# Performance work log

Measured on AMD Instinct MI355X. Metric: run time of the kernel, lower is better.

Reference implementation:

```python
import jax, jax.numpy as jnp
import numpy as np

L, S, B, E, H, M = 1024, 1024, 4, 1024, 16, 256
HD = E // H


def embed_rotary(x, cos, sin):
    # x: (B, T, E); interleaved rotary as in RotaryPositionEncoding.embed_rotary
    x2 = jnp.stack([-x[..., 1::2], x[..., ::2]], axis=-1).reshape(x.shape)
    return x * cos + x2 * sin


def setup_inputs() -> dict:
    key = jax.random.key(0)
    ks = jax.random.split(key, 12)
    return {
        "query": jax.random.normal(ks[0], (L, B, E), jnp.float32),
        "key": jax.random.normal(ks[1], (S, B, E), jnp.float32),
        "value": jax.random.normal(ks[2], (S, B, E), jnp.float32),
        "in_proj_weight": jax.random.normal(ks[3], (3 * E, E), jnp.float32) * (E ** -0.5),
        "in_proj_bias": jax.random.normal(ks[4], (3 * E,), jnp.float32) * 0.02,
        "out_proj_weight": jax.random.normal(ks[5], (E, E), jnp.float32) * (E ** -0.5),
        "out_proj_bias": jax.random.normal(ks[6], (E,), jnp.float32) * 0.02,
        "q_pe": jax.random.uniform(ks[7], (B, L, E, 2), jnp.float32),
        "kv_pe": jax.random.uniform(ks[8], (B, S, E, 2), jnp.float32),
        "k_mem": jax.random.normal(ks[9], (M, B, E), jnp.float32),
        "v_mem": jax.random.normal(ks[10], (M, B, E), jnp.float32),
        "gate_attn": jax.random.normal(ks[11], (H,), jnp.float32),
    }


def reference(query, key, value, in_proj_weight, in_proj_bias, out_proj_weight,
              out_proj_bias, q_pe, kv_pe, k_mem, v_mem, gate_attn):
    scaling = HD ** -0.5
    # separate q/k/v projections from slices of in_proj (q!=k!=v branch)
    q = query @ in_proj_weight[:E].T + in_proj_bias[:E]
    k = key @ in_proj_weight[E:2 * E].T + in_proj_bias[E:2 * E]
    v = value @ in_proj_weight[2 * E:].T + in_proj_bias[2 * E:]
    q = q * scaling
    # rotary PE applied on (B, T, E) layout
    q = embed_rotary(q.swapaxes(0, 1), q_pe[..., 0], q_pe[..., 1]).swapaxes(0, 1)
    k = embed_rotary(k.swapaxes(0, 1), kv_pe[..., 0], kv_pe[..., 1]).swapaxes(0, 1)
    # (T, B, E) -> (B*H, T, HD)
    qh = q.reshape(L, B * H, HD).swapaxes(0, 1)
    kh = k.reshape(S, B * H, HD).swapaxes(0, 1)
    vh = v.reshape(S, B * H, HD).swapaxes(0, 1)
    scores = jnp.einsum('bld,bsd->bls', qh, kh)  # (B*H, L, S)
    # slot-competition: softmax over queries, renormalize over keys
    w = jax.nn.softmax(scores, axis=-2) + 1e-8
    w = w / jnp.sum(w, axis=-1, keepdims=True)
    attn = jnp.einsum('bls,bsd->bld', w, vh)
    # memory attention (k_mem/v_mem already projected, shape (M, B, E))
    kmh = k_mem.reshape(M, B * H, HD).swapaxes(0, 1)
    vmh = v_mem.reshape(M, B * H, HD).swapaxes(0, 1)
    wm = jax.nn.softmax(jnp.einsum('bld,bmd->blm', qh, kmh), axis=-1)
    attn_mem = jnp.einsum('blm,bmd->bld', wm, vmh)
    # per-head sigmoid gating between memory and main outputs
    gate = jnp.tile(jax.nn.sigmoid(gate_attn), B)[:, None, None]  # (B*H,1,1)
    attn = gate * attn_mem + (1.0 - gate) * attn
    out = attn.swapaxes(0, 1).reshape(L, B, E) @ out_proj_weight.T + out_proj_bias
    return out
```

## Files before the change

### kernel.cpp

```cpp
#include <hip/hip_runtime.h>
#include <hip/hip_bf16.h>

typedef __bf16 bf16;
typedef __bf16 bf16x8 __attribute__((ext_vector_type(8)));
typedef float f32x4 __attribute__((ext_vector_type(4)));

#define LL 1024
#define SS 1024
#define BB 4
#define EE 1024
#define HH 16
#define MM 256
#define HD 64
#define BH 64

__device__ __forceinline__ f32x4 mfma16(bf16x8 a, bf16x8 b, f32x4 c) {
  return __builtin_amdgcn_mfma_f32_16x16x32_bf16(a, b, c, 0, 0, 0);
}

__device__ __forceinline__ void gload_lds16(const bf16* g, bf16* l) {
  __builtin_amdgcn_global_load_lds(
      (const __attribute__((address_space(1))) unsigned int*)(g),
      (__attribute__((address_space(3))) unsigned int*)(l), 16, 0, 0);
}

#define RING_BARRIER(N)                                         \
  do {                                                          \
    asm volatile("s_waitcnt vmcnt(" #N ")" ::: "memory");       \
    __builtin_amdgcn_s_barrier();                               \
    __builtin_amdgcn_sched_barrier(0);                          \
  } while (0)

__device__ __forceinline__ bf16x8 cvt8(const float* p) {
  const f32x4 lo = *reinterpret_cast<const f32x4*>(p);
  const f32x4 hi = *reinterpret_cast<const f32x4*>(p + 4);
  bf16x8 r;
  r[0] = (bf16)lo[0]; r[1] = (bf16)lo[1]; r[2] = (bf16)lo[2]; r[3] = (bf16)lo[3];
  r[4] = (bf16)hi[0]; r[5] = (bf16)hi[1]; r[6] = (bf16)hi[2]; r[7] = (bf16)hi[3];
  return r;
}

__global__ __launch_bounds__(256) void cvt_all_kernel(
    const float* __restrict__ ipw, const float* __restrict__ opw,
    const float* __restrict__ k_mem, const float* __restrict__ query,
    const float* __restrict__ key_i, const float* __restrict__ value,
    bf16* __restrict__ wb, bf16* __restrict__ opwb, bf16* __restrict__ kmemb,
    bf16* __restrict__ xq, bf16* __restrict__ xk, bf16* __restrict__ xv) {
  const int bid = blockIdx.x, tid = threadIdx.x;
  if (bid >= 6656) {
    const size_t i8 = ((size_t)(bid - 6656) * 256 + tid) * 8;
    const int e = (int)(i8 & (EE - 1));
    const int row = (int)(i8 >> 10);
    const int s = row >> 2, b = row & 3;
    *reinterpret_cast<bf16x8*>(xv + (((size_t)b * SS + s) << 10) + e) = cvt8(value + i8);
    return;
  }
  const float* src; bf16* dst; int base;
  if (bid < 1536)      { src = ipw;   dst = wb;    base = 0; }
  else if (bid < 2048) { src = opw;   dst = opwb;  base = 1536; }
  else if (bid < 2560) { src = k_mem; dst = kmemb; base = 2048; }
  else if (bid < 4608) { src = query; dst = xq;    base = 2560; }
  else                 { src = key_i; dst = xk;    base = 4608; }
  const size_t i = ((size_t)(bid - base) * 256 + tid) * 8;
  *reinterpret_cast<bf16x8*>(dst + i) = cvt8(src + i);
}

__global__ __launch_bounds__(256) void vmt_kernel(
    const float* __restrict__ v_mem, bf16* __restrict__ vmT) {
  __shared__ float sm[64][65];
  const int bid = blockIdx.x;
  const int bh = bid >> 2, mc = bid & 3;
  const int b = bh >> 4, h = bh & 15;
  const int m0 = mc * 64;
  const int tid = threadIdx.x;
  const int d = tid & 63, mi = tid >> 6;
#pragma unroll
  for (int mm = mi; mm < 64; mm += 4)
    sm[mm][d] = v_mem[((size_t)(m0 + mm) * BB + b) * EE + h * 64 + d];
  __syncthreads();
  const int mw = tid & 63, di = tid >> 6;
#pragma unroll
  for (int dd = di; dd < 64; dd += 4)
    vmT[((size_t)bh * HD + dd) * MM + m0 + mw] = (bf16)sm[mw][dd];
}

__global__ __launch_bounds__(256) void rope_kernel(
    bf16* __restrict__ qh, bf16* __restrict__ kh,
    const float* __restrict__ q_pe, const float* __restrict__ kv_pe) {
  const size_t CP = (size_t)BH * LL * HD / 8;
  size_t gi = (size_t)blockIdx.x * 256 + threadIdx.x;
  bf16* x; const float* pe;
  if (gi < CP) { x = qh; pe = q_pe; }
  else         { x = kh; pe = kv_pe; gi -= CP; }
  const int d8 = gi & 7;
  const int t  = (int)((gi >> 3) & (LL - 1));
  const int bh = (int)(gi >> 13);
  const int b = bh >> 4, h = bh & 15;
  bf16* xp = x + gi * 8;
  const float* pp = pe + (((size_t)b * LL + t) * EE + h * 64 + d8 * 8) * 2;
  bf16x8 v = *reinterpret_cast<const bf16x8*>(xp);
  const f32x4 p0 = *reinterpret_cast<const f32x4*>(pp);
  const f32x4 p1 = *reinterpret_cast<const f32x4*>(pp + 4);
  const f32x4 p2 = *reinterpret_cast<const f32x4*>(pp + 8);
  const f32x4 p3 = *reinterpret_cast<const f32x4*>(pp + 12);
  float cs[8], sn[8], xv[8];
  cs[0]=p0[0]; sn[0]=p0[1]; cs[1]=p0[2]; sn[1]=p0[3];
  cs[2]=p1[0]; sn[2]=p1[1]; cs[3]=p1[2]; sn[3]=p1[3];
  cs[4]=p2[0]; sn[4]=p2[1]; cs[5]=p2[2]; sn[5]=p2[3];
  cs[6]=p3[0]; sn[6]=p3[1]; cs[7]=p3[2]; sn[7]=p3[3];
#pragma unroll
  for (int j = 0; j < 8; ++j) xv[j] = (float)v[j];
  bf16x8 o;
#pragma unroll
  for (int j = 0; j < 8; j += 2) {
    o[j]     = (bf16)(xv[j]     * cs[j]     - xv[j + 1] * sn[j]);
    o[j + 1] = (bf16)(xv[j + 1] * cs[j + 1] + xv[j]     * sn[j + 1]);
  }
  *reinterpret_cast<bf16x8*>(xp) = o;
}

__global__ __launch_bounds__(256) void gemm3_kernel(
    const bf16* __restrict__ xq, const bf16* __restrict__ xk,
    const bf16* __restrict__ xv, const bf16* __restrict__ wb,
    const float* __restrict__ ipb, bf16* __restrict__ qh,
    bf16* __restrict__ kh, bf16* __restrict__ vhT) {
  __shared__ bf16 As[3][4096];
  __shared__ bf16 Bs[3][4096];
  const int tid = threadIdx.x;
  const int wv = tid >> 6, lane = tid & 63;
  const int lrow = lane & 15, lkg = lane >> 4;
  const int wr = wv >> 1, wc = wv & 1;
  const int n = (blockIdx.x & 7) * 96 + (blockIdx.x >> 3);
  const int which = n >> 8, sub = n & 255;

  const bf16* X; const bf16* W;
  int rowA0, colB0;
  if (which == 2) {
    X = wb + 2 * (size_t)EE * EE;
    W = xv;
    rowA0 = (sub & 7) * 128;
    colB0 = (sub >> 3) * 128;
  } else {
    X = (which == 0) ? xq : xk;
    W = wb + (size_t)which * EE * EE;
    rowA0 = (sub >> 3) * 128;
    colB0 = (sub & 7) * 128;
  }

  const f32x4 zero = {0.f, 0.f, 0.f, 0.f};
  f32x4 acc[4][4];
#pragma unroll
  for (int i = 0; i < 4; ++i)
#pragma unroll
    for (int j = 0; j < 4; ++j) acc[i][j] = zero;

  auto stage = [&](int buf, int k0) {
#pragma unroll
    for (int t = 0; t < 2; ++t) {
      const int i = wv * 2 + t;
      const int slot = i * 64 + lane;
      const int srow = slot & 127, sk8 = slot >> 7;
      gload_lds16(X + (size_t)(rowA0 + srow) * EE + k0 + sk8 * 8, &As[buf][i * 512]);
      gload_lds16(W + (size_t)(colB0 + srow) * EE + k0 + sk8 * 8, &Bs[buf][i * 512]);
    }
  };

  stage(0, 0);
  stage(1, 32);
  RING_BARRIER(4);
  for (int ks = 0; ks < 32; ++ks) {
    const int buf = ks % 3;
    if (ks + 2 < 32) stage((ks + 2) % 3, (ks + 2) * 32);
    bf16x8 av[4], bv[4];
#pragma unroll
    for (int i = 0; i < 4; ++i) {
      av[i] = *reinterpret_cast<const bf16x8*>(&As[buf][lkg * 1024 + (wr * 64 + i * 16 + lrow) * 8]);
      bv[i] = *reinterpret_cast<const bf16x8*>(&Bs[buf][lkg * 1024 + (wc * 64 + i * 16 + lrow) * 8]);
    }
#pragma unroll
    for (int mt = 0; mt < 4; ++mt)
#pragma unroll
      for (int nt = 0; nt < 4; ++nt)
        acc[mt][nt] = mfma16(av[mt], bv[nt], acc[mt][nt]);
    if (ks + 2 < 32) { RING_BARRIER(4); } else { RING_BARRIER(0); }
  }

  if (which == 2) {
#pragma unroll
    for (int mt = 0; mt < 4; ++mt) {
#pragma unroll
      for (int r = 0; r < 4; ++r) {
        const int rowg = rowA0 + wr * 64 + mt * 16 + lkg * 4 + r;
        const float bs = ipb[2 * EE + rowg];
        const int h = rowg >> 6, d = rowg & 63;
#pragma unroll
        for (int nt = 0; nt < 4; ++nt) {
          const int c = colB0 + wc * 64 + nt * 16 + lrow;
          const int b = c >> 10, s = c & (SS - 1);
          vhT[(((size_t)(b * HH + h)) * HD + d) * SS + s] = (bf16)(acc[mt][nt][r] + bs);
        }
      }
    }
  } else {
#pragma unroll
    for (int nt = 0; nt < 4; ++nt) {
      const int col = colB0 + wc * 64 + nt * 16 + lrow;
      const float bs = ipb[which * EE + col];
      const int h = col >> 6, d = col & 63;
#pragma unroll
      for (int mt = 0; mt < 4; ++mt) {
#pragma unroll
        for (int r = 0; r < 4; ++r) {
          const int rowg = rowA0 + wr * 64 + mt * 16 + lkg * 4 + r;
          const int t = rowg >> 2;
          const int b = rowg & 3;
          float v = acc[mt][nt][r] + bs;
          if (which == 0) v *= 0.125f;
          const int bh = b * HH + h;
          if (which == 1)
            kh[((size_t)bh * LL + t) * HD + d] = (bf16)v;
          else
            qh[((size_t)bh * LL + t) * HD + d] = (bf16)v;
        }
      }
    }
  }
}

__global__ __launch_bounds__(256) void gemm_out_kernel(
    const bf16* __restrict__ Xb, const bf16* __restrict__ W,
    const float* __restrict__ bias, float* __restrict__ outf) {
  __shared__ bf16 As[3][4096];
  __shared__ bf16 Bs[3][2048];
  const int tid = threadIdx.x;
  const int wv = tid >> 6, lane = tid & 63;
  const int lrow = lane & 15, lkg = lane >> 4;
  const int wr = wv >> 1, wc = wv & 1;
  const int n = (blockIdx.x & 7) * 64 + (blockIdx.x >> 3);
  const int rowt = n >> 4, colt = n & 15;
  const int rowA0 = rowt * 128, colB0 = colt * 64;

  const f32x4 zero = {0.f, 0.f, 0.f, 0.f};
  f32x4 acc[4][2];
#pragma unroll
  for (int i = 0; i < 4; ++i)
#pragma unroll
    for (int j = 0; j < 2; ++j) acc[i][j] = zero;

  auto stage = [&](int buf, int k0) {
#pragma unroll
    for (int t = 0; t < 2; ++t) {
      const int i = wv * 2 + t;
      const int slot = i * 64 + lane;
      const int srow = slot & 127, sk8 = slot >> 7;
      gload_lds16(Xb + (size_t)(rowA0 + srow) * EE + k0 + sk8 * 8, &As[buf][i * 512]);
    }
    {
      const int slot = wv * 64 + lane;
      const int srow = slot & 63, sk8 = slot >> 6;
      gload_lds16(W + (size_t)(colB0 + srow) * EE + k0 + sk8 * 8, &Bs[buf][wv * 512]);
    }
  };

  stage(0, 0);
  stage(1, 32);
  RING_BARRIER(3);
  for (int ks = 0; ks < 32; ++ks) {
    const int buf = ks % 3;
    if (ks + 2 < 32) stage((ks + 2) % 3, (ks + 2) * 32);
    bf16x8 av[4], bv[2];
#pragma unroll
    for (int i = 0; i < 4; ++i)
      av[i] = *reinterpret_cast<const bf16x8*>(&As[buf][lkg * 1024 + (wr * 64 + i * 16 + lrow) * 8]);
#pragma unroll
    for (int j = 0; j < 2; ++j)
      bv[j] = *reinterpret_cast<const bf16x8*>(&Bs[buf][lkg * 512 + (wc * 32 + j * 16 + lrow) * 8]);
#pragma unroll
    for (int mt = 0; mt < 4; ++mt)
#pragma unroll
      for (int nt = 0; nt < 2; ++nt)
        acc[mt][nt] = mfma16(av[mt], bv[nt], acc[mt][nt]);
    if (ks + 2 < 32) { RING_BARRIER(3); } else { RING_BARRIER(0); }
  }

#pragma unroll
  for (int nt = 0; nt < 2; ++nt) {
    const int col = colB0 + wc * 32 + nt * 16 + lrow;
    const float bs = bias[col];
#pragma unroll
    for (int mt = 0; mt < 4; ++mt)
#pragma unroll
      for (int r = 0; r < 4; ++r) {
        const int rowg = rowA0 + wr * 64 + mt * 16 + lkg * 4 + r;
        outf[(size_t)rowg * EE + col] = acc[mt][nt][r] + bs;
      }
  }
}

__global__ __launch_bounds__(256) void stats_kernel(
    const bf16* __restrict__ qh, const bf16* __restrict__ kh,
    float* __restrict__ moff) {
  __shared__ float sm[4][4][16], sd[4][4][16];
  const int tid = threadIdx.x;
  const int wv = tid >> 6, lane = tid & 63;
  const int lrow = lane & 15, lkg = lane >> 4;
  const int n = blockIdx.x;
  const int j = n >> 3;
  const int bh = (n & 7) + 8 * (j >> 4);
  const int s0 = (j & 15) * 64;

  bf16x8 b0[4], b1[4];
#pragma unroll
  for (int ct = 0; ct < 4; ++ct) {
    const bf16* kp = kh + ((size_t)bh * SS + s0 + ct * 16 + lrow) * HD + lkg * 8;
    b0[ct] = *reinterpret_cast<const bf16x8*>(kp);
    b1[ct] = *reinterpret_cast<const bf16x8*>(kp + 32);
  }

  const f32x4 zero = {0.f, 0.f, 0.f, 0.f};
  float m[4] = {-1e30f, -1e30f, -1e30f, -1e30f};
  float d[4] = {0.f, 0.f, 0.f, 0.f};
  const bf16* qbase = qh + ((size_t)bh * LL + wv * 256 + lrow) * HD + lkg * 8;
  for (int i = 0; i < 16; ++i) {
    bf16x8 a0 = *reinterpret_cast<const bf16x8*>(qbase + (size_t)i * 16 * HD);
    bf16x8 a1 = *reinterpret_cast<const bf16x8*>(qbase + (size_t)i * 16 * HD + 32);
#pragma unroll
    for (int ct = 0; ct < 4; ++ct) {
      f32x4 c = zero;
      c = mfma16(a0, b0[ct], c);
      c = mfma16(a1, b1[ct], c);
      float tm = fmaxf(fmaxf(c[0], c[1]), fmaxf(c[2], c[3]));
      float nm = fmaxf(m[ct], tm);
      float dd = d[ct] * __expf(m[ct] - nm);
#pragma unroll
      for (int r = 0; r < 4; ++r) dd += __expf(c[r] - nm);
      d[ct] = dd; m[ct] = nm;
    }
  }
#pragma unroll
  for (int off = 16; off < 64; off <<= 1) {
#pragma unroll
    for (int ct = 0; ct < 4; ++ct) {
      float mo = __shfl_xor(m[ct], off);
      float dd = __shfl_xor(d[ct], off);
      float nm = fmaxf(m[ct], mo);
      d[ct] = d[ct] * __expf(m[ct] - nm) + dd * __expf(mo - nm);
      m[ct] = nm;
    }
  }
  if (lkg == 0) {
#pragma unroll
    for (int ct = 0; ct < 4; ++ct) { sm[wv][ct][lrow] = m[ct]; sd[wv][ct][lrow] = d[ct]; }
  }
  __syncthreads();
  if (wv == 0 && lkg == 0) {
#pragma unroll
    for (int ct = 0; ct < 4; ++ct) {
      float mm = sm[0][ct][lrow], dd = sd[0][ct][lrow];
#pragma unroll
      for (int w = 1; w < 4; ++w) {
        float mo = sm[w][ct][lrow], d2 = sd[w][ct][lrow];
        float nm = fmaxf(mm, mo);
        dd = dd * __expf(mm - nm) + d2 * __expf(mo - nm);
        mm = nm;
      }
      moff[(size_t)bh * SS + s0 + ct * 16 + lrow] = mm + __logf(dd);
    }
  }
}

__global__ __launch_bounds__(64) void colsum_kernel(
    const bf16* __restrict__ vhT, float* __restrict__ colsum) {
  const int bh = blockIdx.x, d = blockIdx.y, lane = threadIdx.x;
  const bf16* p = vhT + ((size_t)bh * HD + d) * SS;
  float s = 0.f;
  for (int i = lane; i < SS; i += 64) s += (float)p[i];
#pragma unroll
  for (int off = 32; off; off >>= 1) s += __shfl_xor(s, off);
  if (lane == 0) colsum[bh * HD + d] = s;
}

__global__ __launch_bounds__(256) void attn_kernel(
    const bf16* __restrict__ qh, const bf16* __restrict__ kh,
    const bf16* __restrict__ vhT, const bf16* __restrict__ vmT,
    const bf16* __restrict__ k_mem, const float* __restrict__ gate_w,
    const float* __restrict__ moff, const float* __restrict__ colsum,
    bf16* __restrict__ attn2) {
  __shared__ bf16 Ks[3][2048];
  __shared__ bf16 Vs[3][2048];
  __shared__ bf16 wt[4][32][40];
  const int tid = threadIdx.x;
  const int wv = tid >> 6, lane = tid & 63;
  const int lrow = lane & 15, lkg = lane >> 4;
  const int bid = blockIdx.x;
  const int bh = (bid & 7) + 8 * (bid >> 6);
  const int b = bh >> 4, h = bh & 15;
  const int l0 = ((bid >> 3) & 7) * 128 + wv * 32;

  bf16x8 aq[2][2];
#pragma unroll
  for (int rt = 0; rt < 2; ++rt) {
    const bf16* qp = qh + ((size_t)bh * LL + l0 + rt * 16 + lrow) * HD + lkg * 8;
    aq[rt][0] = *reinterpret_cast<const bf16x8*>(qp);
    aq[rt][1] = *reinterpret_cast<const bf16x8*>(qp + 32);
  }

  bf16x8 ones;
#pragma unroll
  for (int i = 0; i < 8; ++i) ones[i] = (bf16)1.0f;

  const f32x4 zero = {0.f, 0.f, 0.f, 0.f};
  f32x4 acc[2][4], accm[2][4], racc[2];
#pragma unroll
  for (int rt = 0; rt < 2; ++rt) {
    racc[rt] = zero;
#pragma unroll
    for (int i = 0; i < 4; ++i) { acc[rt][i] = zero; accm[rt][i] = zero; }
  }

  const int srow = lane & 31, sk8h = lane >> 5;
  auto stageK = [&](int buf, int s0) {
    gload_lds16(kh + ((size_t)bh * SS + s0 + srow) * HD + (wv * 2 + sk8h) * 8,
                &Ks[buf][wv * 512]);
  };
  auto stageV = [&](int buf, int s0) {
    gload_lds16(vhT + ((size_t)bh * HD + lane) * SS + s0 + wv * 8,
                &Vs[buf][wv * 512]);
  };
  auto stageKM = [&](int buf, int m0) {
    gload_lds16(k_mem + ((size_t)(m0 + srow) * BB + b) * EE + h * 64 + (wv * 2 + sk8h) * 8,
                &Ks[buf][wv * 512]);
  };
  auto stageVM = [&](int buf, int m0) {
    gload_lds16(vmT + ((size_t)bh * HD + lane) * MM + m0 + wv * 8,
                &Vs[buf][wv * 512]);
  };
  auto kfrag = [&](int buf, int t, int half) {
    return *reinterpret_cast<const bf16x8*>(&Ks[buf][((half * 4 + lkg) * 32 + t * 16 + lrow) * 8]);
  };
  auto vfrag = [&](int buf, int dt) {
    return *reinterpret_cast<const bf16x8*>(&Vs[buf][(lkg * 64 + dt * 16 + lrow) * 8]);
  };

  stageK(0, 0); stageV(0, 0);
  stageK(1, 32); stageV(1, 32);
  RING_BARRIER(2);
  for (int s0 = 0; s0 < SS; s0 += 32) {
    const int idx = s0 >> 5;
    const int buf = idx % 3;
    if (s0 + 64 < SS) { stageK((idx + 2) % 3, s0 + 64); stageV((idx + 2) % 3, s0 + 64); }
    bf16x8 kf[2][2];
#pragma unroll
    for (int t = 0; t < 2; ++t) { kf[t][0] = kfrag(buf, t, 0); kf[t][1] = kfrag(buf, t, 1); }
    f32x4 sc[2][2];
#pragma unroll
    for (int rt = 0; rt < 2; ++rt)
#pragma unroll
      for (int t = 0; t < 2; ++t) {
        f32x4 c = zero;
        c = mfma16(aq[rt][0], kf[t][0], c);
        c = mfma16(aq[rt][1], kf[t][1], c);
        sc[rt][t] = c;
      }
#pragma unroll
    for (int t = 0; t < 2; ++t) {
      const float mo = moff[(size_t)bh * SS + s0 + t * 16 + lrow];
#pragma unroll
      for (int rt = 0; rt < 2; ++rt)
#pragma unroll
        for (int r = 0; r < 4; ++r)
          wt[wv][rt * 16 + lkg * 4 + r][t * 16 + lrow] = (bf16)__expf(sc[rt][t][r] - mo);
    }
    bf16x8 aw[2];
#pragma unroll
    for (int rt = 0; rt < 2; ++rt) {
      aw[rt] = *reinterpret_cast<const bf16x8*>(&wt[wv][rt * 16 + lrow][lkg * 8]);
      racc[rt] = mfma16(aw[rt], ones, racc[rt]);
    }
#pragma unroll
    for (int dt = 0; dt < 4; ++dt) {
      bf16x8 bv = vfrag(buf, dt);
#pragma unroll
      for (int rt = 0; rt < 2; ++rt) acc[rt][dt] = mfma16(aw[rt], bv, acc[rt][dt]);
    }
    if (s0 + 64 < SS) { RING_BARRIER(2); } else { RING_BARRIER(0); }
  }

  float mx[2][4], dn[2][4];
#pragma unroll
  for (int rt = 0; rt < 2; ++rt)
#pragma unroll
    for (int r = 0; r < 4; ++r) { mx[rt][r] = -1e30f; dn[rt][r] = 0.f; }
  stageKM(0, 0);
  stageKM(1, 32);
  RING_BARRIER(1);
  for (int m0 = 0; m0 < MM; m0 += 32) {
    const int idx = m0 >> 5;
    const int buf = idx % 3;
    if (m0 + 64 < MM) stageKM((idx + 2) % 3, m0 + 64);
    bf16x8 kf[2][2];
#pragma unroll
    for (int t = 0; t < 2; ++t) { kf[t][0] = kfrag(buf, t, 0); kf[t][1] = kfrag(buf, t, 1); }
#pragma unroll
    for (int rt = 0; rt < 2; ++rt)
#pragma unroll
      for (int t = 0; t < 2; ++t) {
        f32x4 c = zero;
        c = mfma16(aq[rt][0], kf[t][0], c);
        c = mfma16(aq[rt][1], kf[t][1], c);
#pragma unroll
        for (int r = 0; r < 4; ++r) {
          float nm = fmaxf(mx[rt][r], c[r]);
          dn[rt][r] = dn[rt][r] * __expf(mx[rt][r] - nm) + __expf(c[r] - nm);
          mx[rt][r] = nm;
        }
      }
    if (m0 + 64 < MM) { RING_BARRIER(1); } else { RING_BARRIER(0); }
  }
#pragma unroll
  for (int off = 1; off < 16; off <<= 1) {
#pragma unroll
    for (int rt = 0; rt < 2; ++rt)
#pragma unroll
      for (int r = 0; r < 4; ++r) {
        float mo = __shfl_xor(mx[rt][r], off);
        float dd = __shfl_xor(dn[rt][r], off);
        float nm = fmaxf(mx[rt][r], mo);
        dn[rt][r] = dn[rt][r] * __expf(mx[rt][r] - nm) + dd * __expf(mo - nm);
        mx[rt][r] = nm;
      }
  }
#pragma unroll
  for (int rt = 0; rt < 2; ++rt)
#pragma unroll
    for (int r = 0; r < 4; ++r) dn[rt][r] = 1.f / dn[rt][r];

  stageKM(0, 0); stageVM(0, 0);
  stageKM(1, 32); stageVM(1, 32);
  RING_BARRIER(2);
  for (int m0 = 0; m0 < MM; m0 += 32) {
    const int idx = m0 >> 5;
    const int buf = idx % 3;
    if (m0 + 64 < MM) { stageKM((idx + 2) % 3, m0 + 64); stageVM((idx + 2) % 3, m0 + 64); }
    bf16x8 kf[2][2];
#pragma unroll
    for (int t = 0; t < 2; ++t) { kf[t][0] = kfrag(buf, t, 0); kf[t][1] = kfrag(buf, t, 1); }
#pragma unroll
    for (int rt = 0; rt < 2; ++rt)
#pragma unroll
      for (int t = 0; t < 2; ++t) {
        f32x4 c = zero;
        c = mfma16(aq[rt][0], kf[t][0], c);
        c = mfma16(aq[rt][1], kf[t][1], c);
#pragma unroll
        for (int r = 0; r < 4; ++r)
          wt[wv][rt * 16 + lkg * 4 + r][t * 16 + lrow] = (bf16)(__expf(c[r] - mx[rt][r]) * dn[rt][r]);
      }
    bf16x8 aw[2];
#pragma unroll
    for (int rt = 0; rt < 2; ++rt)
      aw[rt] = *reinterpret_cast<const bf16x8*>(&wt[wv][rt * 16 + lrow][lkg * 8]);
#pragma unroll
    for (int dt = 0; dt < 4; ++dt) {
      bf16x8 bv = vfrag(buf, dt);
#pragma unroll
      for (int rt = 0; rt < 2; ++rt) accm[rt][dt] = mfma16(aw[rt], bv, accm[rt][dt]);
    }
    if (m0 + 64 < MM) { RING_BARRIER(2); } else { RING_BARRIER(0); }
  }

  float g = gate_w[h];
  g = 1.f / (1.f + __expf(-g));

#pragma unroll
  for (int dt = 0; dt < 4; ++dt) {
    const int d = dt * 16 + lrow;
    const float cv = colsum[bh * HD + d] * 1e-8f;
#pragma unroll
    for (int rt = 0; rt < 2; ++rt)
#pragma unroll
      for (int r = 0; r < 4; ++r) {
        const int lg = l0 + rt * 16 + lkg * 4 + r;
        const float den = racc[rt][r] + (float)SS * 1e-8f;
        const float amain = (acc[rt][dt][r] + cv) / den;
        const float v = g * accm[rt][dt][r] + (1.f - g) * amain;
        attn2[((size_t)lg * BB + b) * EE + h * 64 + d] = (bf16)v;
      }
  }
}

extern "C" void kernel_launch(void* const* d_in, const int* in_sizes, int n_in,
                              void* d_out, int out_size, void* d_ws, size_t ws_size,
                              hipStream_t stream) {
  const float* query = (const float*)d_in[0];
  const float* key_i = (const float*)d_in[1];
  const float* value = (const float*)d_in[2];
  const float* ipw   = (const float*)d_in[3];
  const float* ipb   = (const float*)d_in[4];
  const float* opw   = (const float*)d_in[5];
  const float* opb   = (const float*)d_in[6];
  const float* q_pe  = (const float*)d_in[7];
  const float* kv_pe = (const float*)d_in[8];
  const float* k_mem = (const float*)d_in[9];
  const float* v_mem = (const float*)d_in[10];
  const float* gate  = (const float*)d_in[11];

  char* ws = (char*)d_ws;
  bf16* qh    = (bf16*)(ws);
  bf16* kh    = (bf16*)(ws + (8u << 20));
  bf16* vhT   = (bf16*)(ws + (16u << 20));
  bf16* attn2 = (bf16*)(ws + (24u << 20));
  bf16* vmT   = (bf16*)(ws + (32u << 20));
  float* moff   = (float*)(ws + (34u << 20));
  float* colsum = (float*)(ws + (34u << 20) + (1u << 18));
  bf16* wb    = (bf16*)(ws + (35u << 20));
  bf16* opwb  = (bf16*)(ws + (41u << 20));
  bf16* kmemb = (bf16*)(ws + (43u << 20));
  bf16* xq = attn2;
  bf16* xk = (bf16*)d_out;
  bf16* xv = (bf16*)d_out + (size_t)SS * BB * EE;

  dim3 blk(256);
  hipLaunchKernelGGL(cvt_all_kernel, dim3(8704), blk, 0, stream, ipw, opw, k_mem,
                     query, key_i, value, wb, opwb, kmemb, xq, xk, xv);
  hipLaunchKernelGGL(vmt_kernel, dim3(256), blk, 0, stream, v_mem, vmT);
  hipLaunchKernelGGL(gemm3_kernel, dim3(768), blk, 0, stream, xq, xk, xv, wb,
                     ipb, qh, kh, vhT);
  hipLaunchKernelGGL(rope_kernel, dim3(4096), blk, 0, stream, qh, kh, q_pe, kv_pe);
  hipLaunchKernelGGL(stats_kernel, dim3(1024), blk, 0, stream, qh, kh, moff);
  hipLaunchKernelGGL(colsum_kernel, dim3(64, 64), dim3(64), 0, stream, vhT, colsum);
  hipLaunchKernelGGL(attn_kernel, dim3(512), blk, 0, stream, qh, kh, vhT, vmT,
                     kmemb, gate, moff, colsum, attn2);
  hipLaunchKernelGGL(gemm_out_kernel, dim3(512), blk, 0, stream, attn2, opwb, opb,
                     (float*)d_out);
}
```

Before: 227.8 us.

## Retile QKV projection GEMM to 256x256 tiles with phased double-buffer pipeline

```diff
diff --git a/kernel.cpp b/kernel.cpp
--- a/kernel.cpp
+++ b/kernel.cpp
@@ -119,102 +119,138 @@
   *reinterpret_cast<bf16x8*>(xp) = o;
 }
 
-__global__ __launch_bounds__(256) void gemm3_kernel(
+__global__ __launch_bounds__(512, 2) void gemm3_kernel(
     const bf16* __restrict__ xq, const bf16* __restrict__ xk,
     const bf16* __restrict__ xv, const bf16* __restrict__ wb,
     const float* __restrict__ ipb, bf16* __restrict__ qh,
     bf16* __restrict__ kh, bf16* __restrict__ vhT) {
-  __shared__ bf16 As[3][4096];
-  __shared__ bf16 Bs[3][4096];
+  __shared__ bf16 Lds[2][2][2][8192];
   const int tid = threadIdx.x;
   const int wv = tid >> 6, lane = tid & 63;
   const int lrow = lane & 15, lkg = lane >> 4;
-  const int wr = wv >> 1, wc = wv & 1;
-  const int n = (blockIdx.x & 7) * 96 + (blockIdx.x >> 3);
-  const int which = n >> 8, sub = n & 255;
-
-  const bf16* X; const bf16* W;
+  const int wr = wv >> 2;
+  const int wc = wv & 3;
+  const int hb = wc >> 1;
+  const int cb = (wc & 1) * 64;
+
+  const int n = (blockIdx.x & 7) * 24 + (blockIdx.x >> 3);
+  const int which = n >> 6, sub = n & 63;
+
+  const bf16* Ap; const bf16* Bp;
   int rowA0, colB0;
   if (which == 2) {
-    X = wb + 2 * (size_t)EE * EE;
-    W = xv;
-    rowA0 = (sub & 7) * 128;
-    colB0 = (sub >> 3) * 128;
+    Ap = wb + 2 * (size_t)EE * EE;
+    Bp = xv;
+    rowA0 = (sub >> 4) * 256;
+    colB0 = (sub & 15) * 256;
   } else {
-    X = (which == 0) ? xq : xk;
-    W = wb + (size_t)which * EE * EE;
-    rowA0 = (sub >> 3) * 128;
-    colB0 = (sub & 7) * 128;
+    Ap = (which == 0) ? xq : xk;
+    Bp = wb + (size_t)which * EE * EE;
+    rowA0 = (sub >> 2) * 256;
+    colB0 = (sub & 3) * 256;
   }
 
   const f32x4 zero = {0.f, 0.f, 0.f, 0.f};
-  f32x4 acc[4][4];
-#pragma unroll
-  for (int i = 0; i < 4; ++i)
+  f32x4 acc[8][4];
+#pragma unroll
+  for (int i = 0; i < 8; ++i)
 #pragma unroll
     for (int j = 0; j < 4; ++j) acc[i][j] = zero;
 
-  auto stage = [&](int buf, int k0) {
-#pragma unroll
-    for (int t = 0; t < 2; ++t) {
-      const int i = wv * 2 + t;
-      const int slot = i * 64 + lane;
-      const int srow = slot & 127, sk8 = slot >> 7;
-      gload_lds16(X + (size_t)(rowA0 + srow) * EE + k0 + sk8 * 8, &As[buf][i * 512]);
-      gload_lds16(W + (size_t)(colB0 + srow) * EE + k0 + sk8 * 8, &Bs[buf][i * 512]);
-    }
-  };
-
-  stage(0, 0);
-  stage(1, 32);
-  RING_BARRIER(4);
-  for (int ks = 0; ks < 32; ++ks) {
-    const int buf = ks % 3;
-    if (ks + 2 < 32) stage((ks + 2) % 3, (ks + 2) * 32);
-    bf16x8 av[4], bv[4];
-#pragma unroll
-    for (int i = 0; i < 4; ++i) {
-      av[i] = *reinterpret_cast<const bf16x8*>(&As[buf][lkg * 1024 + (wr * 64 + i * 16 + lrow) * 8]);
-      bv[i] = *reinterpret_cast<const bf16x8*>(&Bs[buf][lkg * 1024 + (wc * 64 + i * 16 + lrow) * 8]);
-    }
-#pragma unroll
-    for (int mt = 0; mt < 4; ++mt)
-#pragma unroll
-      for (int nt = 0; nt < 4; ++nt)
-        acc[mt][nt] = mfma16(av[mt], bv[nt], acc[mt][nt]);
-    if (ks + 2 < 32) { RING_BARRIER(4); } else { RING_BARRIER(0); }
-  }
+  auto stageHT = [&](int buf, int mat, int half, int kt) {
+    const bf16* src = mat ? Bp : Ap;
+    const int rb = (mat ? colB0 : rowA0) + half * 128;
+#pragma unroll
+    for (int r2 = 0; r2 < 2; ++r2) {
+      const int slot0 = r2 * 512 + wv * 64;
+      const int sl = slot0 + lane;
+      gload_lds16(src + (size_t)(rb + (sl & 127)) * EE + kt * 64 + (sl >> 7) * 8,
+                  &Lds[buf][mat][half][slot0 * 8]);
+    }
+  };
+
+  bf16x8 bvr[4][2];
+
+#define GPHASE(TB, MP, STAGE, VMC)                                             \
+  {                                                                            \
+    if ((MP) == 0) {                                                           \
+      _Pragma("unroll") for (int n_ = 0; n_ < 4; ++n_)                         \
+        _Pragma("unroll") for (int kh_ = 0; kh_ < 2; ++kh_)                    \
+          bvr[n_][kh_] = *reinterpret_cast<const bf16x8*>(                     \
+              &Lds[TB][1][hb][((kh_ * 4 + lkg) * 128 + cb + n_ * 16 + lrow) * 8]); \
+    }                                                                          \
+    bf16x8 av_[2][2];                                                          \
+    _Pragma("unroll") for (int ml_ = 0; ml_ < 2; ++ml_)                        \
+      _Pragma("unroll") for (int kh_ = 0; kh_ < 2; ++kh_)                      \
+        av_[ml_][kh_] = *reinterpret_cast<const bf16x8*>(                      \
+            &Lds[TB][0][wr][((kh_ * 4 + lkg) * 128 + ((MP) * 2 + ml_) * 16 + lrow) * 8]); \
+    STAGE;                                                                     \
+    VMC;                                                                       \
+    __builtin_amdgcn_s_barrier();                                              \
+    asm volatile("s_waitcnt lgkmcnt(0)" ::: "memory");                         \
+    __builtin_amdgcn_sched_barrier(0);                                         \
+    __builtin_amdgcn_s_setprio(1);                                             \
+    _Pragma("unroll") for (int kh_ = 0; kh_ < 2; ++kh_)                        \
+      _Pragma("unroll") for (int ml_ = 0; ml_ < 2; ++ml_)                      \
+        _Pragma("unroll") for (int n_ = 0; n_ < 4; ++n_)                       \
+          acc[(MP) * 2 + ml_][n_] =                                            \
+              mfma16(av_[ml_][kh_], bvr[n_][kh_], acc[(MP) * 2 + ml_][n_]);    \
+    __builtin_amdgcn_s_setprio(0);                                             \
+    __builtin_amdgcn_s_barrier();                                              \
+  }
+
+  stageHT(0, 1, 0, 0); stageHT(0, 1, 1, 0);
+  stageHT(0, 0, 0, 0); stageHT(0, 0, 1, 0);
+  stageHT(1, 1, 0, 1); stageHT(1, 1, 1, 1);
+  asm volatile("s_waitcnt vmcnt(4)" ::: "memory");
+  __builtin_amdgcn_s_barrier();
+
+  for (int j = 0; j < 8; ++j) {
+    const int kt1 = 2 * j + 1, kt2 = 2 * j + 2, kt3 = 2 * j + 3;
+    GPHASE(0, 0, stageHT(1, 0, 0, kt1), (void)0);
+    GPHASE(0, 1, stageHT(1, 0, 1, kt1), (void)0);
+    GPHASE(0, 2, if (kt2 < 16) stageHT(0, 1, 0, kt2), (void)0);
+    GPHASE(0, 3, if (kt2 < 16) stageHT(0, 1, 1, kt2),
+           if (j < 7) { asm volatile("s_waitcnt vmcnt(4)" ::: "memory"); }
+           else       { asm volatile("s_waitcnt vmcnt(0)" ::: "memory"); });
+    GPHASE(1, 0, if (kt2 < 16) stageHT(0, 0, 0, kt2), (void)0);
+    GPHASE(1, 1, if (kt2 < 16) stageHT(0, 0, 1, kt2), (void)0);
+    GPHASE(1, 2, if (kt3 < 16) stageHT(1, 1, 0, kt3), (void)0);
+    GPHASE(1, 3, if (kt3 < 16) stageHT(1, 1, 1, kt3),
+           asm volatile("s_waitcnt vmcnt(4)" ::: "memory"));
+  }
+#undef GPHASE
 
   if (which == 2) {
 #pragma unroll
-    for (int mt = 0; mt < 4; ++mt) {
+    for (int m = 0; m < 8; ++m) {
 #pragma unroll
       for (int r = 0; r < 4; ++r) {
-        const int rowg = rowA0 + wr * 64 + mt * 16 + lkg * 4 + r;
+        const int rowg = rowA0 + wr * 128 + m * 16 + lkg * 4 + r;
         const float bs = ipb[2 * EE + rowg];
         const int h = rowg >> 6, d = rowg & 63;
 #pragma unroll
-        for (int nt = 0; nt < 4; ++nt) {
-          const int c = colB0 + wc * 64 + nt * 16 + lrow;
+        for (int nn = 0; nn < 4; ++nn) {
+          const int c = colB0 + wc * 64 + nn * 16 + lrow;
           const int b = c >> 10, s = c & (SS - 1);
-          vhT[(((size_t)(b * HH + h)) * HD + d) * SS + s] = (bf16)(acc[mt][nt][r] + bs);
+          vhT[(((size_t)(b * HH + h)) * HD + d) * SS + s] = (bf16)(acc[m][nn][r] + bs);
         }
       }
     }
   } else {
 #pragma unroll
-    for (int nt = 0; nt < 4; ++nt) {
-      const int col = colB0 + wc * 64 + nt * 16 + lrow;
+    for (int nn = 0; nn < 4; ++nn) {
+      const int col = colB0 + wc * 64 + nn * 16 + lrow;
       const float bs = ipb[which * EE + col];
       const int h = col >> 6, d = col & 63;
 #pragma unroll
-      for (int mt = 0; mt < 4; ++mt) {
+      for (int m = 0; m < 8; ++m) {
 #pragma unroll
         for (int r = 0; r < 4; ++r) {
-          const int rowg = rowA0 + wr * 64 + mt * 16 + lkg * 4 + r;
+          const int rowg = rowA0 + wr * 128 + m * 16 + lkg * 4 + r;
           const int t = rowg >> 2;
           const int b = rowg & 3;
-          float v = acc[mt][nt][r] + bs;
+          float v = acc[m][nn][r] + bs;
           if (which == 0) v *= 0.125f;
           const int bh = b * HH + h;
           if (which == 1)
@@ -624,7 +660,7 @@
   hipLaunchKernelGGL(cvt_all_kernel, dim3(8704), blk, 0, stream, ipw, opw, k_mem,
                      query, key_i, value, wb, opwb, kmemb, xq, xk, xv);
   hipLaunchKernelGGL(vmt_kernel, dim3(256), blk, 0, stream, v_mem, vmT);
-  hipLaunchKernelGGL(gemm3_kernel, dim3(768), blk, 0, stream, xq, xk, xv, wb,
+  hipLaunchKernelGGL(gemm3_kernel, dim3(192), dim3(512), 0, stream, xq, xk, xv, wb,
                      ipb, qh, kh, vhT);
   hipLaunchKernelGGL(rope_kernel, dim3(4096), blk, 0, stream, qh, kh, q_pe, kv_pe);
   hipLaunchKernelGGL(stats_kernel, dim3(1024), blk, 0, stream, qh, kh, moff);
```

New measurement: 202.5 us. 11.1% less time.
